# Performance work log

Hardware: AMD Instinct MI355X
Metric: run time of the kernel (lower is better)

## Reference

```python
import jax, jax.numpy as jnp
import numpy as np

BEAM = 3
MAX_LENGTH = 32
START = 1


def setup_inputs() -> dict:
    key = jax.random.key(0)
    ks = jax.random.split(key, 10)
    B, S, H, E, V = 32, 64, 512, 256, 32000
    sE = 1.0 / np.sqrt(E)
    sH = 1.0 / np.sqrt(H)
    return {
        "encoder_outputs": jax.random.normal(ks[0], (B, S, H), jnp.float32),
        "encoder_hidden": jax.random.normal(ks[1], (B, H), jnp.float32),
        "emb": jax.random.normal(ks[2], (V, E), jnp.float32) * 0.02,
        "W_ih": jax.random.uniform(ks[3], (3 * H, E), jnp.float32, -sE, sE),
        "W_hh": jax.random.uniform(ks[4], (3 * H, H), jnp.float32, -sH, sH),
        "b_ih": jax.random.uniform(ks[5], (3 * H,), jnp.float32, -sH, sH),
        "b_hh": jax.random.uniform(ks[6], (3 * H,), jnp.float32, -sH, sH),
        "W_out": jax.random.uniform(ks[7], (V, H), jnp.float32, -sH, sH),
        "b_out": jax.random.uniform(ks[8], (V,), jnp.float32, -sH, sH),
    }


def _gru_cell(x, h, W_ih, W_hh, b_ih, b_hh):
    # PyTorch GRU cell math. x: (N,E), h: (N,H)
    gi = x @ W_ih.T + b_ih          # (N, 3H)
    gh = h @ W_hh.T + b_hh          # (N, 3H)
    i_r, i_z, i_n = jnp.split(gi, 3, axis=-1)
    h_r, h_z, h_n = jnp.split(gh, 3, axis=-1)
    r = jax.nn.sigmoid(i_r + h_r)
    z = jax.nn.sigmoid(i_z + h_z)
    n = jnp.tanh(i_n + r * h_n)
    return (1.0 - z) * n + z * h


def reference(encoder_outputs, encoder_hidden, emb, W_ih, W_hh, b_ih, b_hh, W_out, b_out):
    B = encoder_outputs.shape[0]
    K = BEAM
    V, H = W_out.shape
    BK = B * K

    # expand encoder hidden for beams: each batch row repeated K times
    h0 = jnp.repeat(encoder_hidden, K, axis=0)                 # (BK, H)
    tok0 = jnp.full((BK,), START, jnp.int32)
    seqs0 = jnp.full((BK, MAX_LENGTH + 1), START, jnp.int32)   # col 0 = start token
    scores0 = jnp.zeros((BK,), jnp.float32)
    brow = jnp.arange(B)[:, None] * K                          # (B,1)

    def step(carry, t):
        tok, h, seqs, scores = carry
        x = jax.nn.relu(emb[tok])                              # (BK, E) gather + relu
        h_new = _gru_cell(x, h, W_ih, W_hh, b_ih, b_hh)        # (BK, H)
        logits = h_new @ W_out.T + b_out                       # (BK, V)
        logp = jax.nn.log_softmax(logits, axis=-1)
        next_scores, next_tokens = jax.lax.top_k(logp, K)      # (BK, K)
        total = scores.reshape(B, K, 1) + next_scores.reshape(B, K, K)
        top_scores, top_idx = jax.lax.top_k(total.reshape(B, K * K), K)  # (B, K)
        beam_idx = top_idx // K
        tok_idx = top_idx % K
        old = (brow + beam_idx).reshape(-1)                    # (BK,) source beam rows
        new_tok = next_tokens[old, tok_idx.reshape(-1)].astype(jnp.int32)
        h2 = h_new[old]
        seqs2 = jax.lax.dynamic_update_slice(seqs[old], new_tok[:, None], (0, t + 1))
        return (new_tok, h2, seqs2, top_scores.reshape(-1)), None

    (tok, h, seqs, scores), _ = jax.lax.scan(
        step, (tok0, h0, seqs0, scores0), jnp.arange(MAX_LENGTH))

    # beam 0 is best (top_k is sorted descending)
    best_seqs = seqs.reshape(B, K, MAX_LENGTH + 1)[:, 0]       # (B, L+1)
    decoded = jax.nn.one_hot(best_seqs, V, dtype=jnp.float32)  # (B, L+1, V)
    return decoded, h.reshape(B, K, H), scores.reshape(B, K)
```

## Files before the change

kernel.cpp:

```cpp
#include <hip/hip_runtime.h>
#include <float.h>
#include <math.h>


#define BB 32
#define HH 512
#define EE 256
#define VV 32000
#define TSTEPS 32
#define NVCH 63
#define PSTR 64
#define DEC_ELEMS (BB * (TSTEPS + 1) * VV)
#define H_ELEMS (BB * 3 * HH)

__global__ __launch_bounds__(256) void k_transpose_out(
    const float* __restrict__ W, float* __restrict__ Wt) {
  __shared__ float t[32][33];
  const int vb = blockIdx.x * 32;
  const int kb = blockIdx.y * 32;
  const int c = threadIdx.x & 31, rq = threadIdx.x >> 5;
#pragma unroll
  for (int i = 0; i < 4; ++i) {
    int r = rq + i * 8;
    t[r][c] = W[(size_t)(vb + r) * HH + kb + c];
  }
  __syncthreads();
#pragma unroll
  for (int i = 0; i < 4; ++i) {
    int r = rq + i * 8;
    Wt[(size_t)(kb + r) * VV + vb + c] = t[c][r];
  }
}

__global__ __launch_bounds__(256) void k_init(
    const float* __restrict__ enc_h, float* __restrict__ hb0,
    float* __restrict__ scores, int* __restrict__ tok_seq) {
  int idx = blockIdx.x * 256 + threadIdx.x;
  if (idx < BB * HH) hb0[idx] = enc_h[idx];
  if (idx < BB) { scores[idx] = 0.0f; tok_seq[idx] = 1; }
}

template <int KLEN>
__global__ __launch_bounds__(256) void k_gemv(
    const float* __restrict__ Wt,
    const float* __restrict__ hmat,
    float* __restrict__ lpart) {
  __shared__ float hs[32 * KLEN];
  const int tid = threadIdx.x;
  const int vb = blockIdx.x;
  const int kc = blockIdx.y;
  const int k0 = kc * KLEN;

  {
    constexpr int KQ4 = KLEN / 4;
    float4* hd = (float4*)hs;
    const float4* hp = (const float4*)hmat;
    for (int i = tid; i < 32 * KQ4; i += 256) {
      const int r = i / KQ4, off = i % KQ4;
      hd[i] = hp[r * (HH / 4) + (k0 / 4) + off];
    }
  }
  __syncthreads();

  const int v0 = vb * 512 + tid;
  const int v1 = v0 + 256;
  const bool ok1 = (v1 < VV);

  float acc0[32], acc1[32];
#pragma unroll
  for (int r = 0; r < 32; ++r) { acc0[r] = 0.0f; acc1[r] = 0.0f; }

  const float* w0p = Wt + (size_t)k0 * VV + v0;
  const float* w1p = ok1 ? (w0p + 256) : w0p;

  float wa[4], wb[4];
#pragma unroll
  for (int kk = 0; kk < 4; ++kk) {
    wa[kk] = w0p[(size_t)kk * VV];
    wb[kk] = w1p[(size_t)kk * VV];
  }

  for (int kg = 0; kg < KLEN; kg += 4) {
    float na[4], nb[4];
    if (kg + 4 < KLEN) {
      const float* n0 = w0p + (size_t)(kg + 4) * VV;
      const float* n1 = w1p + (size_t)(kg + 4) * VV;
#pragma unroll
      for (int kk = 0; kk < 4; ++kk) {
        na[kk] = n0[(size_t)kk * VV];
        nb[kk] = n1[(size_t)kk * VV];
      }
    }
#pragma unroll
    for (int r = 0; r < 32; ++r) {
      const float4 h4 = *(const float4*)&hs[r * KLEN + kg];
      acc0[r] = fmaf(h4.x, wa[0], acc0[r]);
      acc0[r] = fmaf(h4.y, wa[1], acc0[r]);
      acc0[r] = fmaf(h4.z, wa[2], acc0[r]);
      acc0[r] = fmaf(h4.w, wa[3], acc0[r]);
      acc1[r] = fmaf(h4.x, wb[0], acc1[r]);
      acc1[r] = fmaf(h4.y, wb[1], acc1[r]);
      acc1[r] = fmaf(h4.z, wb[2], acc1[r]);
      acc1[r] = fmaf(h4.w, wb[3], acc1[r]);
    }
    if (kg + 4 < KLEN) {
#pragma unroll
      for (int kk = 0; kk < 4; ++kk) { wa[kk] = na[kk]; wb[kk] = nb[kk]; }
    }
  }

  float* lp = lpart + (size_t)kc * BB * VV;
#pragma unroll
  for (int r = 0; r < 32; ++r) {
    lp[(size_t)r * VV + v0] = acc0[r];
    if (ok1) lp[(size_t)r * VV + v1] = acc1[r];
  }
}

__global__ __launch_bounds__(256) void k_combine(
    const float* __restrict__ lpart, const float* __restrict__ bout,
    float* __restrict__ pm, float* __restrict__ ps, int* __restrict__ pidx,
    const int nkc) {
  const int tid = threadIdx.x;
  const int vb = blockIdx.x;
  const int row = blockIdx.y;
  const int c0 = vb * 512 + tid * 2;
  const bool act = (c0 + 1 < VV);

  float l0 = 0.0f, l1 = 0.0f;
  if (act) {
    for (int kc = 0; kc < nkc; ++kc) {
      const float2 p = *(const float2*)(lpart + ((size_t)kc * BB + row) * VV + c0);
      l0 += p.x; l1 += p.y;
    }
    const float2 b2 = *(const float2*)(bout + c0);
    l0 += b2.x; l1 += b2.y;
  }
  float tm = -FLT_MAX; int ti = 0x7fffffff;
  if (act) {
    tm = l0; ti = c0;
    if (l1 > tm) { tm = l1; ti = c0 + 1; }
  }
#pragma unroll
  for (int off = 1; off < 64; off <<= 1) {
    const float om = __shfl_xor(tm, off);
    const int oi = __shfl_xor(ti, off);
    if (om > tm || (om == tm && oi < ti)) { tm = om; ti = oi; }
  }
  __shared__ float wm[4]; __shared__ int wi[4];
  __shared__ float bm_s; __shared__ int bi_s;
  __shared__ float wsum[4];
  const int wv = tid >> 6, lane = tid & 63;
  if (lane == 0) { wm[wv] = tm; wi[wv] = ti; }
  __syncthreads();
  if (tid == 0) {
    float m = wm[0]; int ii = wi[0];
#pragma unroll
    for (int w = 1; w < 4; ++w) {
      if (wm[w] > m || (wm[w] == m && wi[w] < ii)) { m = wm[w]; ii = wi[w]; }
    }
    bm_s = m; bi_s = ii;
  }
  __syncthreads();
  const float bm = bm_s;
  float sv = act ? (__expf(l0 - bm) + __expf(l1 - bm)) : 0.0f;
#pragma unroll
  for (int off = 1; off < 64; off <<= 1) sv += __shfl_xor(sv, off);
  if (lane == 0) wsum[wv] = sv;
  __syncthreads();
  if (tid == 0) {
    pm[row * PSTR + vb] = bm;
    ps[row * PSTR + vb] = wsum[0] + wsum[1] + wsum[2] + wsum[3];
    pidx[row * PSTR + vb] = bi_s;
  }
}

__global__ __launch_bounds__(256) void k_gru(
    const int step,
    const float* __restrict__ emb,
    const float* __restrict__ W_ih,
    const float* __restrict__ W_hh,
    const float* __restrict__ b_ih, const float* __restrict__ b_hh,
    const float* __restrict__ hin, float* __restrict__ hout,
    const float* __restrict__ pm, const float* __restrict__ ps,
    const int* __restrict__ pidx,
    float* __restrict__ scores, int* __restrict__ tok_seq) {
  const int tid = threadIdx.x;
  const int rg = blockIdx.x >> 4;
  const int jt = blockIdx.x & 15;
  const int r0 = rg * 4, j0 = jt * 32;
  const int lane = tid & 63, wv = tid >> 6;

  __shared__ int toks[4];
  __shared__ float xs[4][EE];
  __shared__ float hsm[4][HH];
  __shared__ float gpart[24 * 272];

  if (step == 0) {
    if (tid < 4) toks[tid] = 1;
  } else {
    const int row = r0 + wv;
    const bool cv = (lane < NVCH);
    const float m = cv ? pm[row * PSTR + lane] : -FLT_MAX;
    const float s = cv ? ps[row * PSTR + lane] : 0.0f;
    const int ix = cv ? pidx[row * PSTR + lane] : 0x7fffffff;
    float gm = m; int gi = ix;
#pragma unroll
    for (int off = 1; off < 64; off <<= 1) {
      const float om = __shfl_xor(gm, off);
      const int oi = __shfl_xor(gi, off);
      if (om > gm || (om == gm && oi < gi)) { gm = om; gi = oi; }
    }
    float term = cv ? s * __expf(m - gm) : 0.0f;
#pragma unroll
    for (int off = 1; off < 64; off <<= 1) term += __shfl_xor(term, off);
    if (lane == 0) {
      toks[wv] = gi;
      if (jt == 0) {
        scores[row] -= logf(term);
        tok_seq[step * BB + row] = gi;
      }
    }
  }
  __syncthreads();
  if (step == TSTEPS) return;

  for (int i = tid; i < 4 * EE; i += 256) {
    const int r = i >> 8, c = i & (EE - 1);
    const float e = emb[(size_t)toks[r] * EE + c];
    xs[r][c] = e > 0.0f ? e : 0.0f;
  }
  for (int i = tid; i < 4 * HH; i += 256) {
    const int r = i >> 9, c = i & (HH - 1);
    hsm[r][c] = hin[(r0 + r) * HH + c];
  }
  __syncthreads();

  const int jh = tid & 31, kq = tid >> 5;
  const int j = j0 + jh;
  float ai[3][4], ah[3][4];
#pragma unroll
  for (int g = 0; g < 3; ++g)
#pragma unroll
    for (int r = 0; r < 4; ++r) { ai[g][r] = 0.0f; ah[g][r] = 0.0f; }

#pragma unroll 2
  for (int q = 0; q < 8; ++q) {
    const int k4 = kq * 32 + q * 4;
    float4 xr[4];
#pragma unroll
    for (int r = 0; r < 4; ++r) xr[r] = *(const float4*)&xs[r][k4];
#pragma unroll
    for (int g = 0; g < 3; ++g) {
      const float4 w = *(const float4*)&W_ih[(size_t)(g * HH + j) * EE + k4];
#pragma unroll
      for (int r = 0; r < 4; ++r) {
        ai[g][r] = fmaf(xr[r].x, w.x, ai[g][r]);
        ai[g][r] = fmaf(xr[r].y, w.y, ai[g][r]);
        ai[g][r] = fmaf(xr[r].z, w.z, ai[g][r]);
        ai[g][r] = fmaf(xr[r].w, w.w, ai[g][r]);
      }
    }
  }
#pragma unroll 2
  for (int q = 0; q < 16; ++q) {
    const int k4 = kq * 64 + q * 4;
    float4 hr[4];
#pragma unroll
    for (int r = 0; r < 4; ++r) hr[r] = *(const float4*)&hsm[r][k4];
#pragma unroll
    for (int g = 0; g < 3; ++g) {
      const float4 w = *(const float4*)&W_hh[(size_t)(g * HH + j) * HH + k4];
#pragma unroll
      for (int r = 0; r < 4; ++r) {
        ah[g][r] = fmaf(hr[r].x, w.x, ah[g][r]);
        ah[g][r] = fmaf(hr[r].y, w.y, ah[g][r]);
        ah[g][r] = fmaf(hr[r].z, w.z, ah[g][r]);
        ah[g][r] = fmaf(hr[r].w, w.w, ah[g][r]);
      }
    }
  }
  {
    const int base = kq * 34 + jh;
#pragma unroll
    for (int g = 0; g < 3; ++g)
#pragma unroll
      for (int r = 0; r < 4; ++r) {
        gpart[(g * 4 + r) * 272 + base] = ai[g][r];
        gpart[(12 + g * 4 + r) * 272 + base] = ah[g][r];
      }
  }
  __syncthreads();

  if (tid < 128) {
    const int r = tid >> 5, jh2 = tid & 31;
    const int j2 = j0 + jh2;
    float g6[6];
#pragma unroll
    for (int c = 0; c < 6; ++c) {
      const int cc = (c < 3) ? (c * 4 + r) : (12 + (c - 3) * 4 + r);
      float s = 0.0f;
#pragma unroll
      for (int q = 0; q < 8; ++q) s += gpart[cc * 272 + q * 34 + jh2];
      g6[c] = s;
    }
    const float ir = g6[0] + b_ih[j2];
    const float iz = g6[1] + b_ih[HH + j2];
    const float in_ = g6[2] + b_ih[2 * HH + j2];
    const float hr_ = g6[3] + b_hh[j2];
    const float hz = g6[4] + b_hh[HH + j2];
    const float hn = g6[5] + b_hh[2 * HH + j2];
    const float rr = 1.0f / (1.0f + expf(-(ir + hr_)));
    const float zz = 1.0f / (1.0f + expf(-(iz + hz)));
    const float nn = tanhf(in_ + rr * hn);
    hout[(r0 + r) * HH + j2] = (1.0f - zz) * nn + zz * hsm[r][j2];
  }
}

__global__ __launch_bounds__(256) void k_out(
    const int* __restrict__ tok_seq, const float* __restrict__ hfin,
    const float* __restrict__ scores, float* __restrict__ out) {
  const int blk = blockIdx.x, tid = threadIdx.x;
  if (blk < BB * (TSTEPS + 1)) {
    const int b = blk / (TSTEPS + 1), t = blk % (TSTEPS + 1);
    const int tok = tok_seq[t * BB + b];
    const int tq = tok >> 2, tl = tok & 3;
    float4* op = (float4*)(out + (size_t)blk * VV);
    for (int i = tid; i < VV / 4; i += 256) {
      float4 z = {0.0f, 0.0f, 0.0f, 0.0f};
      if (i == tq) (&z.x)[tl] = 1.0f;
      op[i] = z;
    }
  } else if (blk < BB * (TSTEPS + 1) + 12) {
#pragma unroll
    for (int it = 0; it < 4; ++it) {
      const int idx = (blk - BB * (TSTEPS + 1)) * 1024 + it * 256 + tid;
      if (idx < H_ELEMS / 4) {
        const int fi = idx * 4;
        const int b = fi / (3 * HH);
        const int j0 = (fi % (3 * HH)) % HH;
        ((float4*)(out + DEC_ELEMS))[idx] =
            *(const float4*)(hfin + b * HH + j0);
      }
    }
  } else {
    if (tid < BB * 3) {
      out[(size_t)DEC_ELEMS + H_ELEMS + tid] = scores[tid / 3];
    }
  }
}

extern "C" void kernel_launch(void* const* d_in, const int* in_sizes, int n_in,
                              void* d_out, int out_size, void* d_ws, size_t ws_size,
                              hipStream_t stream) {
  const float* enc_h = (const float*)d_in[1];
  const float* emb   = (const float*)d_in[2];
  const float* W_ih  = (const float*)d_in[3];
  const float* W_hh  = (const float*)d_in[4];
  const float* b_ih  = (const float*)d_in[5];
  const float* b_hh  = (const float*)d_in[6];
  const float* W_out = (const float*)d_in[7];
  const float* b_out = (const float*)d_in[8];
  float* out = (float*)d_out;

  float* ws = (float*)d_ws;
  float* Wt_out  = ws;
  float* hb0     = Wt_out + 16384000;
  float* hb1     = hb0 + BB * HH;
  float* pm      = hb1 + BB * HH;
  float* ps      = pm + BB * PSTR;
  float* scores  = ps + BB * PSTR;
  int*   pidx    = (int*)(scores + BB);
  int*   tok_seq = pidx + BB * PSTR;
  float* lpart   = (float*)(tok_seq + BB * (TSTEPS + 1));

  const size_t fixed = 16384000 + 2ull * BB * HH + 2ull * BB * PSTR + BB +
                       BB * PSTR + BB * (TSTEPS + 1);
  int nkc = 8;
  if (ws_size < (fixed + 8ull * BB * VV) * 4) nkc = 4;
  if (ws_size < (fixed + 4ull * BB * VV) * 4) nkc = 2;

  k_transpose_out<<<dim3(1000, 16), 256, 0, stream>>>(W_out, Wt_out);
  k_init<<<64, 256, 0, stream>>>(enc_h, hb0, scores, tok_seq);

  for (int t = 0; t < TSTEPS; ++t) {
    float* hin  = (t & 1) ? hb1 : hb0;
    float* hout = (t & 1) ? hb0 : hb1;
    k_gru<<<128, 256, 0, stream>>>(t, emb, W_ih, W_hh, b_ih, b_hh,
                                   hin, hout, pm, ps, pidx, scores, tok_seq);
    if (nkc == 8)
      k_gemv<64><<<dim3(63, 8), 256, 0, stream>>>(Wt_out, hout, lpart);
    else if (nkc == 4)
      k_gemv<128><<<dim3(63, 4), 256, 0, stream>>>(Wt_out, hout, lpart);
    else
      k_gemv<256><<<dim3(63, 2), 256, 0, stream>>>(Wt_out, hout, lpart);
    k_combine<<<dim3(63, BB), 256, 0, stream>>>(lpart, b_out, pm, ps, pidx, nkc);
  }
  k_gru<<<128, 256, 0, stream>>>(TSTEPS, emb, W_ih, W_hh, b_ih, b_hh,
                                 hb0, hb1, pm, ps, pidx, scores, tok_seq);
  k_out<<<BB * (TSTEPS + 1) + 13, 256, 0, stream>>>(tok_seq, hb0, scores, out);
}
```

Baseline: 1.940 ms.

## Fuse output GEMV with softmax partials and drop split-K logits buffer

Replaces the split-K GEMV that wrote full partial logits to global memory, plus the separate combine kernel, with a single fused kernel. Each block computes full-K dot products for 8 rows and 256 vocab columns, adds the bias, and emits per-chunk max, argmax and sum-exp directly. This removes the large partial-logit round trip through memory and one launch per step. In exchange W_out is now read once per 8-row group (4 times per step instead of once) and the work is spread over 500 blocks arranged with XCD-aware indexing. The GRU kernel's merge now reduces 125 chunks, two per lane.

New measurement: 2.350 ms. 21.1% more time.

```diff
diff --git a/kernel.cpp b/kernel.cpp
--- a/kernel.cpp
+++ b/kernel.cpp
@@ -8,8 +8,8 @@
 #define EE 256
 #define VV 32000
 #define TSTEPS 32
-#define NVCH 63
-#define PSTR 64
+#define NCH 125
+#define PSTR 128
 #define DEC_ELEMS (BB * (TSTEPS + 1) * VV)
 #define H_ELEMS (BB * 3 * HH)
 
@@ -40,138 +40,119 @@
   if (idx < BB) { scores[idx] = 0.0f; tok_seq[idx] = 1; }
 }
 
-template <int KLEN>
-__global__ __launch_bounds__(256) void k_gemv(
+__global__ __launch_bounds__(256) void k_gemv_fused(
     const float* __restrict__ Wt,
     const float* __restrict__ hmat,
-    float* __restrict__ lpart) {
-  __shared__ float hs[32 * KLEN];
+    const float* __restrict__ bout,
+    float* __restrict__ pm, float* __restrict__ ps, int* __restrict__ pidx) {
+  const int bid = blockIdx.x;
+  const int xcd = bid & 7, slot = bid >> 3;
+  const int rg = slot & 3;
+  const int vb = (slot >> 2) * 8 + xcd;
+  if (vb >= NCH) return;
   const int tid = threadIdx.x;
-  const int vb = blockIdx.x;
-  const int kc = blockIdx.y;
-  const int k0 = kc * KLEN;
-
+
+  __shared__ float hs[8][HH];
   {
-    constexpr int KQ4 = KLEN / 4;
+    const float4* hp = (const float4*)(hmat + (size_t)rg * 8 * HH);
     float4* hd = (float4*)hs;
-    const float4* hp = (const float4*)hmat;
-    for (int i = tid; i < 32 * KQ4; i += 256) {
-      const int r = i / KQ4, off = i % KQ4;
-      hd[i] = hp[r * (HH / 4) + (k0 / 4) + off];
-    }
-  }
-  __syncthreads();
-
-  const int v0 = vb * 512 + tid;
-  const int v1 = v0 + 256;
-  const bool ok1 = (v1 < VV);
-
-  float acc0[32], acc1[32];
-#pragma unroll
-  for (int r = 0; r < 32; ++r) { acc0[r] = 0.0f; acc1[r] = 0.0f; }
-
-  const float* w0p = Wt + (size_t)k0 * VV + v0;
-  const float* w1p = ok1 ? (w0p + 256) : w0p;
-
-  float wa[4], wb[4];
-#pragma unroll
-  for (int kk = 0; kk < 4; ++kk) {
-    wa[kk] = w0p[(size_t)kk * VV];
-    wb[kk] = w1p[(size_t)kk * VV];
-  }
-
-  for (int kg = 0; kg < KLEN; kg += 4) {
-    float na[4], nb[4];
-    if (kg + 4 < KLEN) {
-      const float* n0 = w0p + (size_t)(kg + 4) * VV;
-      const float* n1 = w1p + (size_t)(kg + 4) * VV;
-#pragma unroll
-      for (int kk = 0; kk < 4; ++kk) {
-        na[kk] = n0[(size_t)kk * VV];
-        nb[kk] = n1[(size_t)kk * VV];
-      }
-    }
-#pragma unroll
-    for (int r = 0; r < 32; ++r) {
-      const float4 h4 = *(const float4*)&hs[r * KLEN + kg];
-      acc0[r] = fmaf(h4.x, wa[0], acc0[r]);
-      acc0[r] = fmaf(h4.y, wa[1], acc0[r]);
-      acc0[r] = fmaf(h4.z, wa[2], acc0[r]);
-      acc0[r] = fmaf(h4.w, wa[3], acc0[r]);
-      acc1[r] = fmaf(h4.x, wb[0], acc1[r]);
-      acc1[r] = fmaf(h4.y, wb[1], acc1[r]);
-      acc1[r] = fmaf(h4.z, wb[2], acc1[r]);
-      acc1[r] = fmaf(h4.w, wb[3], acc1[r]);
-    }
-    if (kg + 4 < KLEN) {
-#pragma unroll
-      for (int kk = 0; kk < 4; ++kk) { wa[kk] = na[kk]; wb[kk] = nb[kk]; }
-    }
-  }
-
-  float* lp = lpart + (size_t)kc * BB * VV;
-#pragma unroll
-  for (int r = 0; r < 32; ++r) {
-    lp[(size_t)r * VV + v0] = acc0[r];
-    if (ok1) lp[(size_t)r * VV + v1] = acc1[r];
-  }
-}
-
-__global__ __launch_bounds__(256) void k_combine(
-    const float* __restrict__ lpart, const float* __restrict__ bout,
-    float* __restrict__ pm, float* __restrict__ ps, int* __restrict__ pidx,
-    const int nkc) {
-  const int tid = threadIdx.x;
-  const int vb = blockIdx.x;
-  const int row = blockIdx.y;
-  const int c0 = vb * 512 + tid * 2;
-  const bool act = (c0 + 1 < VV);
-
-  float l0 = 0.0f, l1 = 0.0f;
-  if (act) {
-    for (int kc = 0; kc < nkc; ++kc) {
-      const float2 p = *(const float2*)(lpart + ((size_t)kc * BB + row) * VV + c0);
-      l0 += p.x; l1 += p.y;
-    }
-    const float2 b2 = *(const float2*)(bout + c0);
-    l0 += b2.x; l1 += b2.y;
-  }
-  float tm = -FLT_MAX; int ti = 0x7fffffff;
-  if (act) {
-    tm = l0; ti = c0;
-    if (l1 > tm) { tm = l1; ti = c0 + 1; }
-  }
-#pragma unroll
-  for (int off = 1; off < 64; off <<= 1) {
-    const float om = __shfl_xor(tm, off);
-    const int oi = __shfl_xor(ti, off);
-    if (om > tm || (om == tm && oi < ti)) { tm = om; ti = oi; }
-  }
-  __shared__ float wm[4]; __shared__ int wi[4];
-  __shared__ float bm_s; __shared__ int bi_s;
-  __shared__ float wsum[4];
-  const int wv = tid >> 6, lane = tid & 63;
-  if (lane == 0) { wm[wv] = tm; wi[wv] = ti; }
-  __syncthreads();
-  if (tid == 0) {
-    float m = wm[0]; int ii = wi[0];
+#pragma unroll
+    for (int i = 0; i < 4; ++i) hd[tid + i * 256] = hp[tid + i * 256];
+  }
+  __syncthreads();
+
+  const int col = vb * 256 + tid;
+  const float* wp = Wt + col;
+
+  float acc[8];
+#pragma unroll
+  for (int r = 0; r < 8; ++r) acc[r] = 0.0f;
+
+  float wc[8];
+#pragma unroll
+  for (int kk = 0; kk < 8; ++kk) wc[kk] = wp[(size_t)kk * VV];
+
+  for (int k0 = 0; k0 < HH; k0 += 8) {
+    float wn[8];
+    const bool more = (k0 + 8 < HH);
+    if (more) {
+      const float* np = wp + (size_t)(k0 + 8) * VV;
+#pragma unroll
+      for (int kk = 0; kk < 8; ++kk) wn[kk] = np[(size_t)kk * VV];
+    }
+#pragma unroll
+    for (int r = 0; r < 8; ++r) {
+      const float4 a = *(const float4*)&hs[r][k0];
+      const float4 b = *(const float4*)&hs[r][k0 + 4];
+      acc[r] = fmaf(a.x, wc[0], acc[r]);
+      acc[r] = fmaf(a.y, wc[1], acc[r]);
+      acc[r] = fmaf(a.z, wc[2], acc[r]);
+      acc[r] = fmaf(a.w, wc[3], acc[r]);
+      acc[r] = fmaf(b.x, wc[4], acc[r]);
+      acc[r] = fmaf(b.y, wc[5], acc[r]);
+      acc[r] = fmaf(b.z, wc[6], acc[r]);
+      acc[r] = fmaf(b.w, wc[7], acc[r]);
+    }
+    if (more) {
+#pragma unroll
+      for (int kk = 0; kk < 8; ++kk) wc[kk] = wn[kk];
+    }
+  }
+
+  const float bo = bout[col];
+#pragma unroll
+  for (int r = 0; r < 8; ++r) acc[r] += bo;
+
+  const int lane = tid & 63, wv = tid >> 6;
+  __shared__ float wm[8][4];
+  __shared__ int wi[8][4];
+  __shared__ float wsm[8][4];
+
+#pragma unroll
+  for (int r = 0; r < 8; ++r) {
+    float tm = acc[r];
+    int ti = col;
+#pragma unroll
+    for (int off = 1; off < 64; off <<= 1) {
+      const float om = __shfl_xor(tm, off);
+      const int oi = __shfl_xor(ti, off);
+      if (om > tm || (om == tm && oi < ti)) { tm = om; ti = oi; }
+    }
+    if (lane == 0) { wm[r][wv] = tm; wi[r][wv] = ti; }
+  }
+  __syncthreads();
+
+  float M[8];
+#pragma unroll
+  for (int r = 0; r < 8; ++r) {
+    const float m0 = fmaxf(wm[r][0], wm[r][1]);
+    const float m1 = fmaxf(wm[r][2], wm[r][3]);
+    M[r] = fmaxf(m0, m1);
+  }
+#pragma unroll
+  for (int r = 0; r < 8; ++r) {
+    float e = __expf(acc[r] - M[r]);
+#pragma unroll
+    for (int off = 1; off < 64; off <<= 1) e += __shfl_xor(e, off);
+    if (lane == 0) wsm[r][wv] = e;
+  }
+  __syncthreads();
+
+  if (tid < 8) {
+    const int r = tid;
+    const int grow = rg * 8 + r;
+    float bmv = wm[r][0];
+    int bix = wi[r][0];
 #pragma unroll
     for (int w = 1; w < 4; ++w) {
-      if (wm[w] > m || (wm[w] == m && wi[w] < ii)) { m = wm[w]; ii = wi[w]; }
-    }
-    bm_s = m; bi_s = ii;
-  }
-  __syncthreads();
-  const float bm = bm_s;
-  float sv = act ? (__expf(l0 - bm) + __expf(l1 - bm)) : 0.0f;
-#pragma unroll
-  for (int off = 1; off < 64; off <<= 1) sv += __shfl_xor(sv, off);
-  if (lane == 0) wsum[wv] = sv;
-  __syncthreads();
-  if (tid == 0) {
-    pm[row * PSTR + vb] = bm;
-    ps[row * PSTR + vb] = wsum[0] + wsum[1] + wsum[2] + wsum[3];
-    pidx[row * PSTR + vb] = bi_s;
+      if (wm[r][w] > bmv || (wm[r][w] == bmv && wi[r][w] < bix)) {
+        bmv = wm[r][w];
+        bix = wi[r][w];
+      }
+    }
+    pm[grow * PSTR + vb] = bmv;
+    ps[grow * PSTR + vb] = wsm[r][0] + wsm[r][1] + wsm[r][2] + wsm[r][3];
+    pidx[grow * PSTR + vb] = bix;
   }
 }
 
@@ -200,18 +181,23 @@
     if (tid < 4) toks[tid] = 1;
   } else {
     const int row = r0 + wv;
-    const bool cv = (lane < NVCH);
-    const float m = cv ? pm[row * PSTR + lane] : -FLT_MAX;
-    const float s = cv ? ps[row * PSTR + lane] : 0.0f;
-    const int ix = cv ? pidx[row * PSTR + lane] : 0x7fffffff;
-    float gm = m; int gi = ix;
+    const float m1 = pm[row * PSTR + lane];
+    const float s1 = ps[row * PSTR + lane];
+    const int i1 = pidx[row * PSTR + lane];
+    const bool c2 = (lane + 64 < NCH);
+    const float m2 = c2 ? pm[row * PSTR + lane + 64] : -FLT_MAX;
+    const float s2 = c2 ? ps[row * PSTR + lane + 64] : 0.0f;
+    const int i2 = c2 ? pidx[row * PSTR + lane + 64] : 0x7fffffff;
+    float gm;
+    int gi;
+    if (m2 > m1) { gm = m2; gi = i2; } else { gm = m1; gi = i1; }
 #pragma unroll
     for (int off = 1; off < 64; off <<= 1) {
       const float om = __shfl_xor(gm, off);
       const int oi = __shfl_xor(gi, off);
       if (om > gm || (om == gm && oi < gi)) { gm = om; gi = oi; }
     }
-    float term = cv ? s * __expf(m - gm) : 0.0f;
+    float term = s1 * __expf(m1 - gm) + (c2 ? s2 * __expf(m2 - gm) : 0.0f);
 #pragma unroll
     for (int off = 1; off < 64; off <<= 1) term += __shfl_xor(term, off);
     if (lane == 0) {
@@ -372,13 +358,6 @@
   float* scores  = ps + BB * PSTR;
   int*   pidx    = (int*)(scores + BB);
   int*   tok_seq = pidx + BB * PSTR;
-  float* lpart   = (float*)(tok_seq + BB * (TSTEPS + 1));
-
-  const size_t fixed = 16384000 + 2ull * BB * HH + 2ull * BB * PSTR + BB +
-                       BB * PSTR + BB * (TSTEPS + 1);
-  int nkc = 8;
-  if (ws_size < (fixed + 8ull * BB * VV) * 4) nkc = 4;
-  if (ws_size < (fixed + 4ull * BB * VV) * 4) nkc = 2;
 
   k_transpose_out<<<dim3(1000, 16), 256, 0, stream>>>(W_out, Wt_out);
   k_init<<<64, 256, 0, stream>>>(enc_h, hb0, scores, tok_seq);
@@ -388,13 +367,7 @@
     float* hout = (t & 1) ? hb0 : hb1;
     k_gru<<<128, 256, 0, stream>>>(t, emb, W_ih, W_hh, b_ih, b_hh,
                                    hin, hout, pm, ps, pidx, scores, tok_seq);
-    if (nkc == 8)
-      k_gemv<64><<<dim3(63, 8), 256, 0, stream>>>(Wt_out, hout, lpart);
-    else if (nkc == 4)
-      k_gemv<128><<<dim3(63, 4), 256, 0, stream>>>(Wt_out, hout, lpart);
-    else
-      k_gemv<256><<<dim3(63, 2), 256, 0, stream>>>(Wt_out, hout, lpart);
-    k_combine<<<dim3(63, BB), 256, 0, stream>>>(lpart, b_out, pm, ps, pidx, nkc);
+    k_gemv_fused<<<512, 256, 0, stream>>>(Wt_out, hout, b_out, pm, ps, pidx);
   }
   k_gru<<<128, 256, 0, stream>>>(TSTEPS, emb, W_ih, W_hh, b_ih, b_hh,
                                  hb0, hb1, pm, ps, pidx, scores, tok_seq);
```
